# Kernel tuning notes

Measured on AMD Instinct MI355X. Metric: run time of the kernel, lower is better.

Reference implementation:

```python
import jax, jax.numpy as jnp
import numpy as np

TEMPERATURE = 1.0
WEIGHT = 1.0


def _transitivity_sum(rel):
    """rel: [N, N] relation probabilities for one (batch, relation) slice.
    Computes sum_{a,b,c} relu(rel[a,b] - rel[a,c] * rel[b,c]) via a scan over c
    (outer product of column c), keeping memory at O(N^2) instead of O(N^3)."""
    def step(acc, col):  # col = rel[:, c], shape [N]
        viol = jax.nn.relu(rel - col[:, None] * col[None, :])  # [N, N]
        return acc + jnp.sum(viol), None
    acc, _ = jax.lax.scan(step, jnp.zeros((), rel.dtype), rel.T)
    return acc


def setup_inputs() -> dict:
    key = jax.random.key(0)
    B, N, R = 2, 512, 4
    relation_logits = jax.random.normal(key, (B, N, N, R), dtype=jnp.float32)
    entity_masks = jnp.ones((B, N), dtype=jnp.int32)
    return {"relation_logits": relation_logits, "entity_masks": entity_masks}


def reference(relation_logits, entity_masks):
    B, N, _, R = relation_logits.shape
    probs = jax.nn.sigmoid(relation_logits / TEMPERATURE)  # [B, N, N, R]
    m = (entity_masks > 0).astype(probs.dtype)             # [B, N]
    rel = probs * m[:, :, None, None] * m[:, None, :, None]
    # flatten (batch, relation) and vmap the per-matrix cubic reduction
    rel_br = jnp.transpose(rel, (0, 3, 1, 2)).reshape(B * R, N, N)
    per = jax.vmap(_transitivity_sum)(rel_br)              # [B*R]
    # per-batch loss = sum_r / R; final = weight * mean over batch
    return WEIGHT * jnp.sum(per) / (R * B)
```

## Files before the change

### kernel.cpp

```cpp
#include <hip/hip_runtime.h>
#include <math.h>

#define N      512
#define RNUM   4
#define BNUM   2
#define NSLICE (RNUM * BNUM)
#define TILE   128
#define CT     64
#define PAD    4
#define STRIDE (TILE + PAD)
#define CSPLIT 4
#define NCOLB  16
#define SCALE  0.0625f

__device__ __forceinline__ float sigmoidf_(float x) {
  return 1.0f / (1.0f + __expf(-x));
}

__global__ void zero_out_kernel(float* out) { out[0] = 0.0f; }

__global__ __launch_bounds__(256) void prep_kernel(const float* __restrict__ logits,
                                                   const int* __restrict__ masks,
                                                   float* __restrict__ P,
                                                   float* __restrict__ out) {
  if (blockIdx.x == 0 && threadIdx.x == 0) out[0] = 0.0f;
  int t = blockIdx.x * 256 + threadIdx.x;
  int b = t / (N * N);
  int rem = t - b * (N * N);
  int i = rem / N;
  int j = rem - i * N;
  float4 lg = *(const float4*)(logits + (size_t)t * 4);
  float mm = ((masks[b * N + i] > 0) && (masks[b * N + j] > 0)) ? 1.0f : 0.0f;
  size_t base = (size_t)b * RNUM * N * N + rem;
  P[base + 0 * (size_t)N * N] = mm * sigmoidf_(lg.x);
  P[base + 1 * (size_t)N * N] = mm * sigmoidf_(lg.y);
  P[base + 2 * (size_t)N * N] = mm * sigmoidf_(lg.z);
  P[base + 3 * (size_t)N * N] = mm * sigmoidf_(lg.w);
}

template <bool USE_P>
__global__ __launch_bounds__(256, 2) void work_kernel(const float* __restrict__ P,
                                                      const float* __restrict__ logits,
                                                      const int* __restrict__ masks,
                                                      float* __restrict__ out) {
  __shared__ __align__(16) float tA[CT][STRIDE];
  __shared__ __align__(16) float tB[CT][STRIDE];
  __shared__ float wsum[4];

  const int tid = threadIdx.x;
  const int bid = blockIdx.x;

  if (bid < NCOLB) {
    const int s    = bid >> 1;
    const int half = bid & 1;
    const int c    = half * 256 + tid;
    const int bb   = s >> 2;
    const int r    = s & 3;
    float sum = 0.0f;
    if (USE_P) {
      const float* Ps = P + (size_t)s * N * N + c;
#pragma unroll 8
      for (int a = 0; a < N; ++a) sum += Ps[(size_t)a * N];
    } else {
      const int* mrow = masks + bb * N;
      float mc = (mrow[c] > 0) ? 1.0f : 0.0f;
#pragma unroll 4
      for (int a = 0; a < N; ++a) {
        float ma = (mrow[a] > 0) ? 1.0f : 0.0f;
        size_t idx = ((size_t)(bb * N + a) * N + c) * RNUM + r;
        sum += sigmoidf_(logits[idx]) * ma * mc;
      }
    }
    float v = sum * ((float)N - sum);
    for (int off = 32; off > 0; off >>= 1) v += __shfl_down(v, off, 64);
    const int wid = tid >> 6;
    if ((tid & 63) == 0) wsum[wid] = v;
    __syncthreads();
    if (tid == 0)
      atomicAdd(out, (wsum[0] + wsum[1] + wsum[2] + wsum[3]) * SCALE);
    return;
  }

  const int m  = bid - NCOLB;
  const int bt = m & 3;
  const int at = (m >> 2) & 3;
  const int s  = (m >> 4) & 7;
  const int cz = m >> 7;
  const int a0 = at * TILE;
  const int b0 = bt * TILE;
  const int bb = s >> 2;
  const int r  = s & 3;
  const int cbeg = cz * (N / CSPLIT);
  const int cend = cbeg + (N / CSPLIT);

  const int ta = tid & 15;
  const int tb = tid >> 4;

  const float* Ps = P + (size_t)s * N * N;
  const int* mrow = masks + bb * N;

  float rab[8][8];
  if (USE_P) {
#pragma unroll
    for (int x = 0; x < 8; ++x) {
      int ra = a0 + ((x >> 2) << 6) + ta * 4 + (x & 3);
      float4 r0 = *(const float4*)(Ps + (size_t)ra * N + b0 + tb * 4);
      float4 r1 = *(const float4*)(Ps + (size_t)ra * N + b0 + 64 + tb * 4);
      rab[x][0] = r0.x; rab[x][1] = r0.y; rab[x][2] = r0.z; rab[x][3] = r0.w;
      rab[x][4] = r1.x; rab[x][5] = r1.y; rab[x][6] = r1.z; rab[x][7] = r1.w;
    }
  } else {
#pragma unroll
    for (int x = 0; x < 8; ++x) {
      int ra = a0 + ((x >> 2) << 6) + ta * 4 + (x & 3);
      float ma = (mrow[ra] > 0) ? 1.0f : 0.0f;
#pragma unroll
      for (int y = 0; y < 8; ++y) {
        int cbcol = b0 + ((y >> 2) << 6) + tb * 4 + (y & 3);
        float mb = (mrow[cbcol] > 0) ? 1.0f : 0.0f;
        size_t idx = ((size_t)(bb * N + ra) * N + cbcol) * RNUM + r;
        rab[x][y] = sigmoidf_(logits[idx]) * ma * mb;
      }
    }
  }

  float acc[8][2];
#pragma unroll
  for (int x = 0; x < 8; ++x) { acc[x][0] = 0.0f; acc[x][1] = 0.0f; }

  for (int c0 = cbeg; c0 < cend; c0 += CT) {
    __syncthreads();
    if (USE_P) {
#pragma unroll
      for (int it = 0; it < 8; ++it) {
        int f  = it * 256 + tid;
        int c4 = f & 15;
        int i  = f >> 4;
        int pc = ((((i >> 2) ^ c4) & 31) << 2) | (i & 3);
        float4 va = *(const float4*)(Ps + (size_t)(a0 + i) * N + c0 + c4 * 4);
        tA[c4 * 4 + 0][pc] = va.x;
        tA[c4 * 4 + 1][pc] = va.y;
        tA[c4 * 4 + 2][pc] = va.z;
        tA[c4 * 4 + 3][pc] = va.w;
        float4 vb = *(const float4*)(Ps + (size_t)(b0 + i) * N + c0 + c4 * 4);
        tB[c4 * 4 + 0][pc] = vb.x;
        tB[c4 * 4 + 1][pc] = vb.y;
        tB[c4 * 4 + 2][pc] = vb.z;
        tB[c4 * 4 + 3][pc] = vb.w;
      }
    } else {
#pragma unroll
      for (int it = 0; it < 32; ++it) {
        int e = it * 256 + tid;
        int c = e & 63;
        int i = e >> 6;
        int c4 = (c & 31) >> 2;
        int pc = ((((i >> 2) ^ ((c >> 2) & 31)) & 31) << 2) | (i & 3);
        (void)c4;
        float mc = (mrow[c0 + c] > 0) ? 1.0f : 0.0f;
        {
          float mi = (mrow[a0 + i] > 0) ? 1.0f : 0.0f;
          size_t idx = ((size_t)(bb * N + a0 + i) * N + (c0 + c)) * RNUM + r;
          tA[c][pc] = sigmoidf_(logits[idx]) * mi * mc;
        }
        {
          float mi = (mrow[b0 + i] > 0) ? 1.0f : 0.0f;
          size_t idx = ((size_t)(bb * N + b0 + i) * N + (c0 + c)) * RNUM + r;
          tB[c][pc] = sigmoidf_(logits[idx]) * mi * mc;
        }
      }
    }
    __syncthreads();

#pragma unroll 2
    for (int cg = 0; cg < CT / 4; ++cg) {
      const float* pa = &tA[cg * 4][((ta ^ cg) & 31) << 2];
      const float* pb = &tB[cg * 4][((tb ^ cg) & 31) << 2];
#pragma unroll
      for (int dc = 0; dc < 4; ++dc) {
        float4 a0v = *(const float4*)(pa + dc * STRIDE);
        float4 a1v = *(const float4*)(pa + dc * STRIDE + 64);
        float4 b0v = *(const float4*)(pb + dc * STRIDE);
        float4 b1v = *(const float4*)(pb + dc * STRIDE + 64);
        float av[8] = {a0v.x, a0v.y, a0v.z, a0v.w, a1v.x, a1v.y, a1v.z, a1v.w};
        float bv[8] = {b0v.x, b0v.y, b0v.z, b0v.w, b1v.x, b1v.y, b1v.z, b1v.w};
#pragma unroll
        for (int x = 0; x < 8; ++x) {
#pragma unroll
          for (int y = 0; y < 4; ++y) {
            float t = fmaf(-av[x], bv[y], rab[x][y]);
            acc[x][0] += fabsf(t);
          }
#pragma unroll
          for (int y = 4; y < 8; ++y) {
            float t = fmaf(-av[x], bv[y], rab[x][y]);
            acc[x][1] += fabsf(t);
          }
        }
      }
    }
  }

  float tsum = 0.0f;
#pragma unroll
  for (int x = 0; x < 8; ++x) tsum += acc[x][0] + acc[x][1];

  for (int off = 32; off > 0; off >>= 1) tsum += __shfl_down(tsum, off, 64);

  const int wid = tid >> 6;
  if ((tid & 63) == 0) wsum[wid] = tsum;
  __syncthreads();
  if (tid == 0)
    atomicAdd(out, (wsum[0] + wsum[1] + wsum[2] + wsum[3]) * SCALE);
}

extern "C" void kernel_launch(void* const* d_in, const int* in_sizes, int n_in,
                              void* d_out, int out_size, void* d_ws, size_t ws_size,
                              hipStream_t stream) {
  const float* logits = (const float*)d_in[0];
  const int*   masks  = (const int*)d_in[1];
  float*       out    = (float*)d_out;

  const size_t P_BYTES = (size_t)NSLICE * N * N * sizeof(float);
  const int nblocks = NCOLB + (N / TILE) * (N / TILE) * NSLICE * CSPLIT;

  if (ws_size >= P_BYTES) {
    float* P = (float*)d_ws;
    prep_kernel<<<(BNUM * N * N) / 256, 256, 0, stream>>>(logits, masks, P, out);
    work_kernel<true><<<nblocks, 256, 0, stream>>>(P, logits, masks, out);
  } else {
    zero_out_kernel<<<1, 1, 0, stream>>>(out);
    work_kernel<false><<<nblocks, 256, 0, stream>>>(nullptr, logits, masks, out);
  }
}
```

Measured before the change: 139.1 us.

## Store probabilities in fp16 and use packed half2 math with fdot2 accumulation

The prep kernel now writes the sigmoid probabilities as fp16, which halves the workspace traffic. The main cubic loop computes rab - a*b with packed half2 operations, takes the absolute value with a bitmask, and accumulates into fp32 through fdot2 against ones. The column-chunk size drops to 32 and CSPLIT doubles to 8 so the grid has more blocks, and the LDS staging becomes a simple transposed scatter. This roughly doubles ALU throughput per instruction, but half-precision rounding in the |x| sum may break accuracy tolerance.

```diff
diff --git a/kernel.cpp b/kernel.cpp
--- a/kernel.cpp
+++ b/kernel.cpp
@@ -6,45 +6,185 @@
 #define BNUM   2
 #define NSLICE (RNUM * BNUM)
 #define TILE   128
-#define CT     64
-#define PAD    4
-#define STRIDE (TILE + PAD)
-#define CSPLIT 4
+#define CT     32
+#define LSTR   136
+#define CSPLIT 8
 #define NCOLB  16
 #define SCALE  0.0625f
 
+typedef _Float16 half2_t __attribute__((ext_vector_type(2)));
+
+__device__ __forceinline__ unsigned int h2u(half2_t h) {
+  return __builtin_bit_cast(unsigned int, h);
+}
+__device__ __forceinline__ half2_t u2h(unsigned int u) {
+  return __builtin_bit_cast(half2_t, u);
+}
+
+#if __has_builtin(__builtin_amdgcn_fdot2)
+__device__ __forceinline__ float fdot2_(half2_t a, half2_t b, float c) {
+  return __builtin_amdgcn_fdot2(a, b, c, false);
+}
+#else
+__device__ __forceinline__ float fdot2_(half2_t a, half2_t b, float c) {
+  return c + (float)a.x * (float)b.x + (float)a.y * (float)b.y;
+}
+#endif
+
 __device__ __forceinline__ float sigmoidf_(float x) {
   return 1.0f / (1.0f + __expf(-x));
 }
 
 __global__ void zero_out_kernel(float* out) { out[0] = 0.0f; }
 
-__global__ __launch_bounds__(256) void prep_kernel(const float* __restrict__ logits,
-                                                   const int* __restrict__ masks,
-                                                   float* __restrict__ P,
-                                                   float* __restrict__ out) {
+__global__ __launch_bounds__(256) void prep_f16_kernel(const float* __restrict__ logits,
+                                                       const int* __restrict__ masks,
+                                                       _Float16* __restrict__ P,
+                                                       float* __restrict__ out) {
   if (blockIdx.x == 0 && threadIdx.x == 0) out[0] = 0.0f;
   int t = blockIdx.x * 256 + threadIdx.x;
-  int b = t / (N * N);
-  int rem = t - b * (N * N);
-  int i = rem / N;
-  int j = rem - i * N;
+  int b = t >> 18;
+  int rem = t & (N * N - 1);
+  int i = rem >> 9;
+  int j = rem & (N - 1);
   float4 lg = *(const float4*)(logits + (size_t)t * 4);
   float mm = ((masks[b * N + i] > 0) && (masks[b * N + j] > 0)) ? 1.0f : 0.0f;
   size_t base = (size_t)b * RNUM * N * N + rem;
-  P[base + 0 * (size_t)N * N] = mm * sigmoidf_(lg.x);
-  P[base + 1 * (size_t)N * N] = mm * sigmoidf_(lg.y);
-  P[base + 2 * (size_t)N * N] = mm * sigmoidf_(lg.z);
-  P[base + 3 * (size_t)N * N] = mm * sigmoidf_(lg.w);
-}
-
-template <bool USE_P>
-__global__ __launch_bounds__(256, 2) void work_kernel(const float* __restrict__ P,
-                                                      const float* __restrict__ logits,
-                                                      const int* __restrict__ masks,
-                                                      float* __restrict__ out) {
-  __shared__ __align__(16) float tA[CT][STRIDE];
-  __shared__ __align__(16) float tB[CT][STRIDE];
+  P[base + 0 * (size_t)N * N] = (_Float16)(mm * sigmoidf_(lg.x));
+  P[base + 1 * (size_t)N * N] = (_Float16)(mm * sigmoidf_(lg.y));
+  P[base + 2 * (size_t)N * N] = (_Float16)(mm * sigmoidf_(lg.z));
+  P[base + 3 * (size_t)N * N] = (_Float16)(mm * sigmoidf_(lg.w));
+}
+
+__global__ __launch_bounds__(256, 2) void work_f16_kernel(const _Float16* __restrict__ P,
+                                                          float* __restrict__ out) {
+  __shared__ _Float16 tA[CT][LSTR];
+  __shared__ _Float16 tB[CT][LSTR];
+  __shared__ float wsum[4];
+
+  const int tid = threadIdx.x;
+  const int bid = blockIdx.x;
+
+  if (bid < NCOLB) {
+    const int s    = bid >> 1;
+    const int half = bid & 1;
+    const int c    = half * 256 + tid;
+    const _Float16* col = P + (size_t)s * N * N + c;
+    float sum = 0.0f;
+#pragma unroll 8
+    for (int a = 0; a < N; ++a) sum += (float)col[(size_t)a * N];
+    float v = sum * ((float)N - sum);
+    for (int off = 32; off > 0; off >>= 1) v += __shfl_down(v, off, 64);
+    const int wid = tid >> 6;
+    if ((tid & 63) == 0) wsum[wid] = v;
+    __syncthreads();
+    if (tid == 0)
+      atomicAdd(out, (wsum[0] + wsum[1] + wsum[2] + wsum[3]) * SCALE);
+    return;
+  }
+
+  const int m  = bid - NCOLB;
+  const int bt = m & 3;
+  const int at = (m >> 2) & 3;
+  const int s  = (m >> 4) & 7;
+  const int cz = m >> 7;
+  const int a0 = at * TILE;
+  const int b0 = bt * TILE;
+  const int cbeg = cz * (N / CSPLIT);
+  const int cend = cbeg + (N / CSPLIT);
+
+  const int ta = tid & 15;
+  const int tb = tid >> 4;
+
+  const _Float16* Ph = P + (size_t)s * N * N;
+
+  half2_t rab2[8][4];
+#pragma unroll
+  for (int x = 0; x < 8; ++x) {
+    int ga = a0 + ((x >> 2) << 6) + ta * 4 + (x & 3);
+    uint2 u0 = *(const uint2*)(Ph + (size_t)ga * N + b0 + tb * 4);
+    uint2 u1 = *(const uint2*)(Ph + (size_t)ga * N + b0 + 64 + tb * 4);
+    rab2[x][0] = u2h(u0.x); rab2[x][1] = u2h(u0.y);
+    rab2[x][2] = u2h(u1.x); rab2[x][3] = u2h(u1.y);
+  }
+
+  float acc[8];
+#pragma unroll
+  for (int x = 0; x < 8; ++x) acc[x] = 0.0f;
+
+  const half2_t kOne = {(_Float16)1.0f, (_Float16)1.0f};
+
+  const int sx   = tid & 127;
+  const int sarr = tid >> 7;
+  const _Float16* srow = Ph + (size_t)((sarr ? b0 : a0) + sx) * N;
+  _Float16* dcol = sarr ? &tB[0][sx] : &tA[0][sx];
+
+  for (int c0 = cbeg; c0 < cend; c0 += CT) {
+    __syncthreads();
+    {
+      const uint4* src = (const uint4*)(srow + c0);
+      uint4 q0 = src[0];
+      uint4 q1 = src[1];
+      uint4 q2 = src[2];
+      uint4 q3 = src[3];
+      unsigned int w[16] = {q0.x, q0.y, q0.z, q0.w, q1.x, q1.y, q1.z, q1.w,
+                            q2.x, q2.y, q2.z, q2.w, q3.x, q3.y, q3.z, q3.w};
+      union { unsigned int u32; _Float16 h[2]; } cv;
+#pragma unroll
+      for (int k = 0; k < 16; ++k) {
+        cv.u32 = w[k];
+        dcol[(size_t)(2 * k) * LSTR]     = cv.h[0];
+        dcol[(size_t)(2 * k + 1) * LSTR] = cv.h[1];
+      }
+    }
+    __syncthreads();
+
+#pragma unroll 4
+    for (int c = 0; c < CT; ++c) {
+      uint2 ua0 = *(const uint2*)&tA[c][ta * 4];
+      uint2 ua1 = *(const uint2*)&tA[c][64 + ta * 4];
+      uint2 ub0 = *(const uint2*)&tB[c][tb * 4];
+      uint2 ub1 = *(const uint2*)&tB[c][64 + tb * 4];
+      half2_t av[4] = {u2h(ua0.x), u2h(ua0.y), u2h(ua1.x), u2h(ua1.y)};
+      half2_t bv[4] = {u2h(ub0.x), u2h(ub0.y), u2h(ub1.x), u2h(ub1.y)};
+#pragma unroll
+      for (int x = 0; x < 8; ++x) {
+        _Float16 as = (x & 1) ? av[x >> 1].y : av[x >> 1].x;
+        half2_t asp = {as, as};
+        float a_ = acc[x];
+#pragma unroll
+        for (int yp = 0; yp < 4; ++yp) {
+          half2_t t2 = rab2[x][yp] - asp * bv[yp];
+          half2_t p2 = u2h(h2u(t2) & 0x7FFF7FFFu);
+          a_ = fdot2_(p2, kOne, a_);
+        }
+        acc[x] = a_;
+      }
+    }
+  }
+
+  float tsum = 0.0f;
+#pragma unroll
+  for (int x = 0; x < 8; ++x) tsum += acc[x];
+
+  for (int off = 32; off > 0; off >>= 1) tsum += __shfl_down(tsum, off, 64);
+
+  const int wid = tid >> 6;
+  if ((tid & 63) == 0) wsum[wid] = tsum;
+  __syncthreads();
+  if (tid == 0)
+    atomicAdd(out, (wsum[0] + wsum[1] + wsum[2] + wsum[3]) * SCALE);
+}
+
+#define FCT    64
+#define FSTR   132
+#define FCSPL  4
+
+__global__ __launch_bounds__(256, 2) void work_f32_fallback(const float* __restrict__ logits,
+                                                            const int* __restrict__ masks,
+                                                            float* __restrict__ out) {
+  __shared__ __align__(16) float tA[FCT][FSTR];
+  __shared__ __align__(16) float tB[FCT][FSTR];
   __shared__ float wsum[4];
 
   const int tid = threadIdx.x;
@@ -56,20 +196,14 @@
     const int c    = half * 256 + tid;
     const int bb   = s >> 2;
     const int r    = s & 3;
+    const int* mrow = masks + bb * N;
+    float mc = (mrow[c] > 0) ? 1.0f : 0.0f;
     float sum = 0.0f;
-    if (USE_P) {
-      const float* Ps = P + (size_t)s * N * N + c;
-#pragma unroll 8
-      for (int a = 0; a < N; ++a) sum += Ps[(size_t)a * N];
-    } else {
-      const int* mrow = masks + bb * N;
-      float mc = (mrow[c] > 0) ? 1.0f : 0.0f;
 #pragma unroll 4
-      for (int a = 0; a < N; ++a) {
-        float ma = (mrow[a] > 0) ? 1.0f : 0.0f;
-        size_t idx = ((size_t)(bb * N + a) * N + c) * RNUM + r;
-        sum += sigmoidf_(logits[idx]) * ma * mc;
-      }
+    for (int a = 0; a < N; ++a) {
+      float ma = (mrow[a] > 0) ? 1.0f : 0.0f;
+      size_t idx = ((size_t)(bb * N + a) * N + c) * RNUM + r;
+      sum += sigmoidf_(logits[idx]) * ma * mc;
     }
     float v = sum * ((float)N - sum);
     for (int off = 32; off > 0; off >>= 1) v += __shfl_down(v, off, 64);
@@ -90,37 +224,24 @@
   const int b0 = bt * TILE;
   const int bb = s >> 2;
   const int r  = s & 3;
-  const int cbeg = cz * (N / CSPLIT);
-  const int cend = cbeg + (N / CSPLIT);
+  const int cbeg = cz * (N / FCSPL);
+  const int cend = cbeg + (N / FCSPL);
 
   const int ta = tid & 15;
   const int tb = tid >> 4;
-
-  const float* Ps = P + (size_t)s * N * N;
   const int* mrow = masks + bb * N;
 
   float rab[8][8];
-  if (USE_P) {
-#pragma unroll
-    for (int x = 0; x < 8; ++x) {
-      int ra = a0 + ((x >> 2) << 6) + ta * 4 + (x & 3);
-      float4 r0 = *(const float4*)(Ps + (size_t)ra * N + b0 + tb * 4);
-      float4 r1 = *(const float4*)(Ps + (size_t)ra * N + b0 + 64 + tb * 4);
-      rab[x][0] = r0.x; rab[x][1] = r0.y; rab[x][2] = r0.z; rab[x][3] = r0.w;
-      rab[x][4] = r1.x; rab[x][5] = r1.y; rab[x][6] = r1.z; rab[x][7] = r1.w;
-    }
-  } else {
-#pragma unroll
-    for (int x = 0; x < 8; ++x) {
-      int ra = a0 + ((x >> 2) << 6) + ta * 4 + (x & 3);
-      float ma = (mrow[ra] > 0) ? 1.0f : 0.0f;
-#pragma unroll
-      for (int y = 0; y < 8; ++y) {
-        int cbcol = b0 + ((y >> 2) << 6) + tb * 4 + (y & 3);
-        float mb = (mrow[cbcol] > 0) ? 1.0f : 0.0f;
-        size_t idx = ((size_t)(bb * N + ra) * N + cbcol) * RNUM + r;
-        rab[x][y] = sigmoidf_(logits[idx]) * ma * mb;
-      }
+#pragma unroll
+  for (int x = 0; x < 8; ++x) {
+    int ra = a0 + ((x >> 2) << 6) + ta * 4 + (x & 3);
+    float ma = (mrow[ra] > 0) ? 1.0f : 0.0f;
+#pragma unroll
+    for (int y = 0; y < 8; ++y) {
+      int cb = b0 + ((y >> 2) << 6) + tb * 4 + (y & 3);
+      float mb = (mrow[cb] > 0) ? 1.0f : 0.0f;
+      size_t idx = ((size_t)(bb * N + ra) * N + cb) * RNUM + r;
+      rab[x][y] = sigmoidf_(logits[idx]) * ma * mb;
     }
   }
 
@@ -128,74 +249,48 @@
 #pragma unroll
   for (int x = 0; x < 8; ++x) { acc[x][0] = 0.0f; acc[x][1] = 0.0f; }
 
-  for (int c0 = cbeg; c0 < cend; c0 += CT) {
-    __syncthreads();
-    if (USE_P) {
-#pragma unroll
-      for (int it = 0; it < 8; ++it) {
-        int f  = it * 256 + tid;
-        int c4 = f & 15;
-        int i  = f >> 4;
-        int pc = ((((i >> 2) ^ c4) & 31) << 2) | (i & 3);
-        float4 va = *(const float4*)(Ps + (size_t)(a0 + i) * N + c0 + c4 * 4);
-        tA[c4 * 4 + 0][pc] = va.x;
-        tA[c4 * 4 + 1][pc] = va.y;
-        tA[c4 * 4 + 2][pc] = va.z;
-        tA[c4 * 4 + 3][pc] = va.w;
-        float4 vb = *(const float4*)(Ps + (size_t)(b0 + i) * N + c0 + c4 * 4);
-        tB[c4 * 4 + 0][pc] = vb.x;
-        tB[c4 * 4 + 1][pc] = vb.y;
-        tB[c4 * 4 + 2][pc] = vb.z;
-        tB[c4 * 4 + 3][pc] = vb.w;
-      }
-    } else {
-#pragma unroll
-      for (int it = 0; it < 32; ++it) {
-        int e = it * 256 + tid;
-        int c = e & 63;
-        int i = e >> 6;
-        int c4 = (c & 31) >> 2;
-        int pc = ((((i >> 2) ^ ((c >> 2) & 31)) & 31) << 2) | (i & 3);
-        (void)c4;
-        float mc = (mrow[c0 + c] > 0) ? 1.0f : 0.0f;
-        {
-          float mi = (mrow[a0 + i] > 0) ? 1.0f : 0.0f;
-          size_t idx = ((size_t)(bb * N + a0 + i) * N + (c0 + c)) * RNUM + r;
-          tA[c][pc] = sigmoidf_(logits[idx]) * mi * mc;
-        }
-        {
-          float mi = (mrow[b0 + i] > 0) ? 1.0f : 0.0f;
-          size_t idx = ((size_t)(bb * N + b0 + i) * N + (c0 + c)) * RNUM + r;
-          tB[c][pc] = sigmoidf_(logits[idx]) * mi * mc;
-        }
+  for (int c0 = cbeg; c0 < cend; c0 += FCT) {
+    __syncthreads();
+#pragma unroll
+    for (int it = 0; it < 32; ++it) {
+      int e = it * 256 + tid;
+      int c = e & 63;
+      int i = e >> 6;
+      int pc = ((((i >> 2) ^ ((c >> 2) & 31)) & 31) << 2) | (i & 3);
+      float mc = (mrow[c0 + c] > 0) ? 1.0f : 0.0f;
+      {
+        float mi = (mrow[a0 + i] > 0) ? 1.0f : 0.0f;
+        size_t idx = ((size_t)(bb * N + a0 + i) * N + (c0 + c)) * RNUM + r;
+        tA[c][pc] = sigmoidf_(logits[idx]) * mi * mc;
+      }
+      {
+        float mi = (mrow[b0 + i] > 0) ? 1.0f : 0.0f;
+        size_t idx = ((size_t)(bb * N + b0 + i) * N + (c0 + c)) * RNUM + r;
+        tB[c][pc] = sigmoidf_(logits[idx]) * mi * mc;
       }
     }
     __syncthreads();
 
 #pragma unroll 2
-    for (int cg = 0; cg < CT / 4; ++cg) {
+    for (int cg = 0; cg < FCT / 4; ++cg) {
       const float* pa = &tA[cg * 4][((ta ^ cg) & 31) << 2];
       const float* pb = &tB[cg * 4][((tb ^ cg) & 31) << 2];
 #pragma unroll
       for (int dc = 0; dc < 4; ++dc) {
-        float4 a0v = *(const float4*)(pa + dc * STRIDE);
-        float4 a1v = *(const float4*)(pa + dc * STRIDE + 64);
-        float4 b0v = *(const float4*)(pb + dc * STRIDE);
-        float4 b1v = *(const float4*)(pb + dc * STRIDE + 64);
-        float av[8] = {a0v.x, a0v.y, a0v.z, a0v.w, a1v.x, a1v.y, a1v.z, a1v.w};
-        float bv[8] = {b0v.x, b0v.y, b0v.z, b0v.w, b1v.x, b1v.y, b1v.z, b1v.w};
+        float4 a0v = *(const float4*)(pa + dc * FSTR);
+        float4 a1v = *(const float4*)(pa + dc * FSTR + 64);
+        float4 b0v = *(const float4*)(pb + dc * FSTR);
+        float4 b1v = *(const float4*)(pb + dc * FSTR + 64);
+        float avv[8] = {a0v.x, a0v.y, a0v.z, a0v.w, a1v.x, a1v.y, a1v.z, a1v.w};
+        float bvv[8] = {b0v.x, b0v.y, b0v.z, b0v.w, b1v.x, b1v.y, b1v.z, b1v.w};
 #pragma unroll
         for (int x = 0; x < 8; ++x) {
 #pragma unroll
-          for (int y = 0; y < 4; ++y) {
-            float t = fmaf(-av[x], bv[y], rab[x][y]);
-            acc[x][0] += fabsf(t);
-          }
-#pragma unroll
-          for (int y = 4; y < 8; ++y) {
-            float t = fmaf(-av[x], bv[y], rab[x][y]);
-            acc[x][1] += fabsf(t);
-          }
+          for (int y = 0; y < 4; ++y)
+            acc[x][0] += fabsf(fmaf(-avv[x], bvv[y], rab[x][y]));
+#pragma unroll
+          for (int y = 4; y < 8; ++y)
+            acc[x][1] += fabsf(fmaf(-avv[x], bvv[y], rab[x][y]));
         }
       }
     }
@@ -204,9 +299,7 @@
   float tsum = 0.0f;
 #pragma unroll
   for (int x = 0; x < 8; ++x) tsum += acc[x][0] + acc[x][1];
-
   for (int off = 32; off > 0; off >>= 1) tsum += __shfl_down(tsum, off, 64);
-
   const int wid = tid >> 6;
   if ((tid & 63) == 0) wsum[wid] = tsum;
   __syncthreads();
@@ -221,15 +314,16 @@
   const int*   masks  = (const int*)d_in[1];
   float*       out    = (float*)d_out;
 
-  const size_t P_BYTES = (size_t)NSLICE * N * N * sizeof(float);
-  const int nblocks = NCOLB + (N / TILE) * (N / TILE) * NSLICE * CSPLIT;
+  const size_t P_BYTES = (size_t)NSLICE * N * N * sizeof(_Float16);
 
   if (ws_size >= P_BYTES) {
-    float* P = (float*)d_ws;
-    prep_kernel<<<(BNUM * N * N) / 256, 256, 0, stream>>>(logits, masks, P, out);
-    work_kernel<true><<<nblocks, 256, 0, stream>>>(P, logits, masks, out);
+    _Float16* P = (_Float16*)d_ws;
+    prep_f16_kernel<<<(BNUM * N * N) / 256, 256, 0, stream>>>(logits, masks, P, out);
+    const int nblocks = NCOLB + 4 * 4 * NSLICE * CSPLIT;
+    work_f16_kernel<<<nblocks, 256, 0, stream>>>(P, out);
   } else {
     zero_out_kernel<<<1, 1, 0, stream>>>(out);
-    work_kernel<false><<<nblocks, 256, 0, stream>>>(nullptr, logits, masks, out);
-  }
-}
+    const int nblocks = NCOLB + 4 * 4 * NSLICE * FCSPL;
+    work_f32_fallback<<<nblocks, 256, 0, stream>>>(logits, masks, out);
+  }
+}
```

Result: faster. 115.8 us (-16.8%).
